# Kernel tuning notes

Hardware: AMD Instinct MI355X
Metric: run time of the kernel (lower is better)

Reference implementation:

```python
import jax, jax.numpy as jnp
import numpy as np

B, S, H, V, MAXLEN = 32, 128, 512, 32000, 64


def setup_inputs() -> dict:
    key = jax.random.key(0)
    ks = jax.random.split(key, 10)
    s = 0.05
    return {
        "word_level_rep": jax.random.normal(ks[0], (B, S, H), jnp.float32),
        "sentence_level_rep": jax.random.normal(ks[1], (B, H), jnp.float32),
        "W2": jax.random.normal(ks[2], (H,), jnp.float32) * s,          # Linear(H,1,bias=False)
        "W4": jax.random.normal(ks[3], (H, 2 * H), jnp.float32) * s,    # Linear(2H,H,bias=False), torch layout [out,in]
        "W_ih": jax.random.normal(ks[4], (4 * H, H), jnp.float32) * s,  # LSTM gates i,f,g,o
        "W_hh": jax.random.normal(ks[5], (4 * H, H), jnp.float32) * s,
        "b_ih": jax.random.normal(ks[6], (4 * H,), jnp.float32) * s,
        "b_hh": jax.random.normal(ks[7], (4 * H,), jnp.float32) * s,
        "W_out": jax.random.normal(ks[8], (V, H), jnp.float32) * s,
        "b_out": jax.random.normal(ks[9], (V,), jnp.float32) * s,
        "max_len": MAXLEN,
    }


def reference(word_level_rep, sentence_level_rep, W2, W4, W_ih, W_hh, b_ih, b_hh, W_out, b_out, max_len):
    b, seq, h_dim = word_level_rep.shape

    def step(carry, _):
        h, c = carry
        # sentence-level attention over a singleton memory bank -> weight == 1
        sent_ctx = sentence_level_rep                                   # [B,H]
        # word-level Bahdanau attention
        scores = jnp.tanh(word_level_rep + h[:, None, :]) @ W2          # [B,S]
        attn = jax.nn.softmax(scores, axis=1)                           # [B,S]
        word_ctx = jnp.einsum('bs,bsh->bh', attn, word_level_rep)       # [B,H]
        x = jnp.tanh(jnp.concatenate([sent_ctx, word_ctx], axis=-1) @ W4.T)  # [B,H]
        # PyTorch LSTM cell: gates order i, f, g, o
        gates = x @ W_ih.T + b_ih + h @ W_hh.T + b_hh                   # [B,4H]
        i, f, g, o = jnp.split(gates, 4, axis=-1)
        c_new = jax.nn.sigmoid(f) * c + jax.nn.sigmoid(i) * jnp.tanh(g)
        h_new = jax.nn.sigmoid(o) * jnp.tanh(c_new)
        out = h_new @ W_out.T + b_out                                   # [B,V]
        return (h_new, c_new), out

    h0 = jnp.zeros((b, h_dim), word_level_rep.dtype)
    c0 = jnp.zeros((b, h_dim), word_level_rep.dtype)
    (h_fin, _), outs = jax.lax.scan(step, (h0, c0), None, length=max_len)
    generated_sequence = jnp.transpose(outs, (1, 0, 2))                 # [B,max_len,V]
    return generated_sequence, h_fin
```

## Files before the change

### kernel.cpp

```cpp
#include <hip/hip_runtime.h>
#include <stdint.h>

typedef unsigned short ushort_t;
typedef unsigned long long ull_t;
typedef __attribute__((ext_vector_type(8))) short bf16x8;
typedef __attribute__((ext_vector_type(8))) unsigned short u16x8;
typedef __attribute__((ext_vector_type(4))) unsigned short u16x4;
typedef __attribute__((ext_vector_type(4))) float f32x4;

#define DEV static __device__ __forceinline__
#define SCOPE_AGENT __HIP_MEMORY_SCOPE_AGENT

DEV unsigned short f2bf(float f) {
  unsigned u = __float_as_uint(f);
  u += 0x7FFFu + ((u >> 16) & 1u);
  return (unsigned short)(u >> 16);
}
DEV float bf2f(unsigned short h) { return __uint_as_float(((unsigned)h) << 16); }
DEV float fast_rcp(float x) { return __builtin_amdgcn_rcpf(x); }
DEV float fast_tanh(float x) { float e = __expf(2.f * x); return (e - 1.f) * fast_rcp(e + 1.f); }
DEV float fast_sigm(float x) { return fast_rcp(1.f + __expf(-x)); }

DEV float wave_sum(float v) {
#pragma unroll
  for (int d = 32; d > 0; d >>= 1) v += __shfl_xor(v, d, 64);
  return v;
}
DEV float wave_max(float v) {
#pragma unroll
  for (int d = 32; d > 0; d >>= 1) v = fmaxf(v, __shfl_xor(v, d, 64));
  return v;
}

DEV void async_g2l(const void* g, void* l) {
  __builtin_amdgcn_global_load_lds((const __attribute__((address_space(1))) void*)g,
                                   (__attribute__((address_space(3))) void*)l, 16, 0, 0);
}

DEV unsigned ld_flag(unsigned* p) { return __hip_atomic_load(p, __ATOMIC_RELAXED, SCOPE_AGENT); }
DEV void st_flag(unsigned* p, unsigned v) { __hip_atomic_store(p, v, __ATOMIC_RELAXED, SCOPE_AGENT); }
DEV ull_t ld_u64(ull_t* p) { return __hip_atomic_load(p, __ATOMIC_RELAXED, SCOPE_AGENT); }
DEV void st_u64(ull_t* p, ull_t v) { __hip_atomic_store(p, v, __ATOMIC_RELAXED, SCOPE_AGENT); }
DEV void release_fence() { __builtin_amdgcn_s_waitcnt(0); }

__global__ void k_f2bf(const float* __restrict__ in, ushort_t* __restrict__ out, int n4) {
  int i = blockIdx.x * blockDim.x + threadIdx.x;
  int st = gridDim.x * blockDim.x;
  for (; i < n4; i += st) {
    f32x4 v = *(const f32x4*)(in + (size_t)i * 4);
    u16x4 o;
    o[0] = f2bf(v[0]); o[1] = f2bf(v[1]); o[2] = f2bf(v[2]); o[3] = f2bf(v[3]);
    *(u16x4*)(out + (size_t)i * 4) = o;
  }
}

__global__ __launch_bounds__(256) void k_initP(
    const float* __restrict__ w, const float* __restrict__ sent,
    const float* __restrict__ W4, ushort_t* __restrict__ P, float* __restrict__ sp)
{
  __shared__ float As2[16 * 68];
  __shared__ float Bs2[16 * 68];
  const int tid = threadIdx.x;
  const int m0 = blockIdx.x * 64, n0 = blockIdx.y * 64;
  const int tm = tid & 15, tn = tid >> 4;
  const bool sent_half = (m0 >= 4096);
  float acc[4][4];
#pragma unroll
  for (int i = 0; i < 4; i++)
#pragma unroll
    for (int j = 0; j < 4; j++) acc[i][j] = 0.f;

  for (int k0 = 0; k0 < 512; k0 += 16) {
#pragma unroll
    for (int i = 0; i < 4; i++) {
      int idx = i * 256 + tid;
      int r = idx >> 4, kk = idx & 15;
      int m = m0 + r;
      float va = 0.f;
      if (m < 4096) va = w[(size_t)m * 512 + k0 + kk];
      else if (m < 4128) va = sent[(m - 4096) * 512 + k0 + kk];
      As2[kk * 68 + r] = va;
      Bs2[kk * 68 + r] = W4[(size_t)(n0 + r) * 1024 + (sent_half ? 0 : 512) + k0 + kk];
    }
    __syncthreads();
#pragma unroll
    for (int k = 0; k < 16; k++) {
      f32x4 av = *(const f32x4*)&As2[k * 68 + tm * 4];
      f32x4 bv = *(const f32x4*)&Bs2[k * 68 + tn * 4];
#pragma unroll
      for (int i = 0; i < 4; i++)
#pragma unroll
        for (int j = 0; j < 4; j++) acc[i][j] = fmaf(av[i], bv[j], acc[i][j]);
    }
    __syncthreads();
  }
#pragma unroll
  for (int i = 0; i < 4; i++) {
    int m = m0 + tm * 4 + i;
    if (m >= 4128) continue;
#pragma unroll
    for (int j = 0; j < 4; j++) {
      int n = n0 + tn * 4 + j;
      if (m < 4096) P[(size_t)m * 512 + n] = f2bf(acc[i][j]);
      else sp[(m - 4096) * 512 + n] = acc[i][j];
    }
  }
}

struct GateS {
  ushort_t XHx[32 * 520];
  float gredf[8 * 512];
  float gates[32 * 17];
  float bias[16];
  float cstate[128];
  ushort_t hs16[128];
};
struct AttnS {
  float hs[512];
  float sps[512];
  float sc[128];
  float attw[128];
  float xpart[1024];
  ushort_t xs16[512];
};

__global__ __launch_bounds__(512) void k_recur(
    const float* __restrict__ W2, const float* __restrict__ W_ih, const float* __restrict__ W_hh,
    const float* __restrict__ b_ih, const float* __restrict__ b_hh,
    const ushort_t* __restrict__ w_bf, const ushort_t* __restrict__ P, const float* __restrict__ sp,
    unsigned* hflag, unsigned* xflag, ull_t* hbuf, ull_t* xbuf,
    ull_t* __restrict__ h_A, float* __restrict__ h_fin)
{
  __shared__ union { GateS g; AttnS a; } sm;
  const int bid = blockIdx.x, tid = threadIdx.x;
  const int wv = tid >> 6, lane = tid & 63;

  if (bid < 128) {
    const int n16 = lane & 15, quad = lane >> 4;
    const int grow = (n16 >> 2) * 512 + (bid << 2) + (n16 & 3);
    if (tid < 128) sm.g.cstate[tid] = 0.f;
    if (tid < 16) {
      int gr = (tid >> 2) * 512 + (bid << 2) + (tid & 3);
      sm.g.bias[tid] = b_ih[gr] + b_hh[gr];
    }
    bf16x8 fih[2], fhh[2];
#pragma unroll
    for (int ks = 0; ks < 2; ks++) {
      int kk = (wv * 2 + ks) * 32 + quad * 8;
      const float* pi = W_ih + (size_t)grow * 512 + kk;
      const float* ph = W_hh + (size_t)grow * 512 + kk;
#pragma unroll
      for (int j = 0; j < 8; j++) {
        fih[ks][j] = (short)f2bf(pi[j]);
        fhh[ks][j] = (short)f2bf(ph[j]);
      }
    }
    __syncthreads();

    for (int t = 0; t < 64; t++) {
      if (t > 0 && tid < 128) {
        while (ld_flag(&hflag[tid]) < (unsigned)t) __builtin_amdgcn_s_sleep(2);
      }
      __syncthreads();
      ull_t* hsrc = hbuf + ((t + 1) & 1) * 4096;
#pragma unroll
      for (int i = 0; i < 8; i++) {
        int fl = i * 512 + tid;
        ull_t v = ld_u64(&hsrc[fl]);
        *(ull_t*)&sm.g.XHx[(fl >> 7) * 520 + (fl & 127) * 4] = v;
      }
      __syncthreads();
      f32x4 acc0 = {0.f, 0.f, 0.f, 0.f}, acc1 = {0.f, 0.f, 0.f, 0.f};
#pragma unroll
      for (int ks = 0; ks < 2; ks++) {
        int kk = (wv * 2 + ks) * 32 + quad * 8;
        bf16x8 a0 = *(const bf16x8*)&sm.g.XHx[n16 * 520 + kk];
        bf16x8 a1 = *(const bf16x8*)&sm.g.XHx[(16 + n16) * 520 + kk];
        acc0 = __builtin_amdgcn_mfma_f32_16x16x32_bf16(a0, fhh[ks], acc0, 0, 0, 0);
        acc1 = __builtin_amdgcn_mfma_f32_16x16x32_bf16(a1, fhh[ks], acc1, 0, 0, 0);
      }
      if (tid < 32) {
        while (ld_flag(&xflag[tid]) < (unsigned)(t + 1)) __builtin_amdgcn_s_sleep(2);
      }
      __syncthreads();
#pragma unroll
      for (int i = 0; i < 8; i++) {
        int fl = i * 512 + tid;
        ull_t v = ld_u64(&xbuf[fl]);
        *(ull_t*)&sm.g.XHx[(fl >> 7) * 520 + (fl & 127) * 4] = v;
      }
      __syncthreads();
#pragma unroll
      for (int ks = 0; ks < 2; ks++) {
        int kk = (wv * 2 + ks) * 32 + quad * 8;
        bf16x8 a0 = *(const bf16x8*)&sm.g.XHx[n16 * 520 + kk];
        bf16x8 a1 = *(const bf16x8*)&sm.g.XHx[(16 + n16) * 520 + kk];
        acc0 = __builtin_amdgcn_mfma_f32_16x16x32_bf16(a0, fih[ks], acc0, 0, 0, 0);
        acc1 = __builtin_amdgcn_mfma_f32_16x16x32_bf16(a1, fih[ks], acc1, 0, 0, 0);
      }
      *(f32x4*)&sm.g.gredf[wv * 512 + lane * 4] = acc0;
      *(f32x4*)&sm.g.gredf[wv * 512 + 256 + lane * 4] = acc1;
      __syncthreads();
      {
        float v = 0.f;
#pragma unroll
        for (int k = 0; k < 8; k++) v += sm.g.gredf[k * 512 + tid];
        int mt = tid >> 8, l = (tid >> 2) & 63, r = tid & 3;
        int batch = mt * 16 + ((l >> 4) << 2) + r;
        int n = l & 15;
        sm.g.gates[batch * 17 + n] = v + sm.g.bias[n];
      }
      __syncthreads();
      if (tid < 128) {
        int bb = tid & 31, hr = tid >> 5;
        float gi = sm.g.gates[bb * 17 + hr];
        float gf = sm.g.gates[bb * 17 + 4 + hr];
        float gg = sm.g.gates[bb * 17 + 8 + hr];
        float go = sm.g.gates[bb * 17 + 12 + hr];
        float cold = sm.g.cstate[(bb << 2) + hr];
        float cn = fast_sigm(gf) * cold + fast_sigm(gi) * fast_tanh(gg);
        float hn = fast_sigm(go) * fast_tanh(cn);
        sm.g.cstate[(bb << 2) + hr] = cn;
        sm.g.hs16[(bb << 2) + hr] = f2bf(hn);
        if (t == 63) h_fin[bb * 512 + (bid << 2) + hr] = hn;
      }
      __syncthreads();
      if (tid < 32) {
        ull_t v = *(const ull_t*)&sm.g.hs16[tid << 2];
        st_u64(&hbuf[(t & 1) * 4096 + tid * 128 + bid], v);
        h_A[((tid << 6) + t) * 128 + bid] = v;
        release_fence();
      }
      __syncthreads();
      if (tid == 0) st_flag(&hflag[bid], (unsigned)(t + 1));
    }
  } else {
    const int b = bid - 128;
    float w2v[8];
#pragma unroll
    for (int j = 0; j < 8; j++) w2v[j] = W2[lane * 8 + j];
    sm.a.sps[tid] = sp[b * 512 + tid];
    __syncthreads();

    for (int t = 0; t < 64; t++) {
      if (t > 0 && tid < 128) {
        while (ld_flag(&hflag[tid]) < (unsigned)t) __builtin_amdgcn_s_sleep(2);
      }
      __syncthreads();
      if (tid < 128) {
        ull_t v = ld_u64(&hbuf[((t + 1) & 1) * 4096 + b * 128 + tid]);
        sm.a.hs[tid * 4 + 0] = bf2f((unsigned short)v);
        sm.a.hs[tid * 4 + 1] = bf2f((unsigned short)(v >> 16));
        sm.a.hs[tid * 4 + 2] = bf2f((unsigned short)(v >> 32));
        sm.a.hs[tid * 4 + 3] = bf2f((unsigned short)(v >> 48));
      }
      __syncthreads();
      float hf[8];
#pragma unroll
      for (int j = 0; j < 8; j++) hf[j] = sm.a.hs[lane * 8 + j];
#pragma unroll
      for (int i = 0; i < 16; i++) {
        int s = wv * 16 + i;
        u16x8 wvv = *(const u16x8*)(w_bf + ((size_t)((b << 7) + s) << 9) + lane * 8);
        float acc = 0.f;
#pragma unroll
        for (int j = 0; j < 8; j++) {
          float v = bf2f(wvv[j]) + hf[j];
          float e = __expf(2.f * v);
          acc = fmaf((e - 1.f) * fast_rcp(e + 1.f), w2v[j], acc);
        }
        acc = wave_sum(acc);
        if (lane == 0) sm.a.sc[s] = acc;
      }
      __syncthreads();
      if (wv == 0) {
        float a0 = sm.a.sc[lane], a1 = sm.a.sc[lane + 64];
        float m = wave_max(fmaxf(a0, a1));
        float e0 = __expf(a0 - m), e1 = __expf(a1 - m);
        float inv = fast_rcp(wave_sum(e0 + e1));
        sm.a.attw[lane] = e0 * inv;
        sm.a.attw[lane + 64] = e1 * inv;
      }
      __syncthreads();
      {
        int half = tid >> 8, rp = tid & 255;
        float a0 = 0.f, a1 = 0.f;
        const ushort_t* Pb = P + (((size_t)(b << 7) + half * 64) << 9) + rp * 2;
#pragma unroll 8
        for (int ss = 0; ss < 64; ss++) {
          float aw = sm.a.attw[half * 64 + ss];
          unsigned pv = *(const unsigned*)&Pb[(size_t)ss << 9];
          a0 = fmaf(aw, bf2f((unsigned short)pv), a0);
          a1 = fmaf(aw, bf2f((unsigned short)(pv >> 16)), a1);
        }
        sm.a.xpart[half * 512 + rp * 2] = a0;
        sm.a.xpart[half * 512 + rp * 2 + 1] = a1;
      }
      __syncthreads();
      {
        float xv = fast_tanh(sm.a.xpart[tid] + sm.a.xpart[512 + tid] + sm.a.sps[tid]);
        sm.a.xs16[tid] = f2bf(xv);
      }
      __syncthreads();
      if (tid < 128) {
        ull_t v = *(const ull_t*)&sm.a.xs16[tid << 2];
        st_u64(&xbuf[b * 128 + tid], v);
        release_fence();
      }
      __syncthreads();
      if (tid == 0) st_flag(&xflag[b], (unsigned)(t + 1));
    }
  }
}

__global__ __launch_bounds__(256) void k_gemm(
    const ushort_t* __restrict__ A, const ushort_t* __restrict__ Bw,
    const float* __restrict__ bias, float* __restrict__ C)
{
  __shared__ ushort_t As[128 * 64];
  __shared__ ushort_t Bs[128 * 64];
  const int tid = threadIdx.x;
  const int wave = tid >> 6, lane = tid & 63;
  const int ln = lane & 15, quad = lane >> 4;
  const int bm = blockIdx.x & 15, bn = blockIdx.x >> 4;
  const int wm = wave & 1, wn = wave >> 1;

  f32x4 acc[4][4];
#pragma unroll
  for (int i = 0; i < 4; i++)
#pragma unroll
    for (int j = 0; j < 4; j++) { acc[i][j][0] = 0.f; acc[i][j][1] = 0.f; acc[i][j][2] = 0.f; acc[i][j][3] = 0.f; }

  for (int kt = 0; kt < 8; kt++) {
    const int k0 = kt * 64;
#pragma unroll
    for (int i = 0; i < 4; i++) {
      int s = i * 256 + tid;
      int r = s >> 3, c = s & 7;
      int cs = c ^ (r & 7);
      async_g2l(A + ((size_t)(bm * 128 + r) << 9) + k0 + (cs << 3), &As[s << 3]);
    }
#pragma unroll
    for (int i = 0; i < 4; i++) {
      int s = i * 256 + tid;
      int r = s >> 3, c = s & 7;
      int cs = c ^ (r & 7);
      async_g2l(Bw + ((size_t)(bn * 128 + r) << 9) + k0 + (cs << 3), &Bs[s << 3]);
    }
    __syncthreads();
#pragma unroll
    for (int ks = 0; ks < 2; ks++) {
      bf16x8 af[4], bfr[4];
      int cc = ks * 4 + quad;
#pragma unroll
      for (int f = 0; f < 4; f++) {
        int ra = wm * 64 + f * 16 + ln;
        af[f] = *(const bf16x8*)&As[((ra << 3) + (cc ^ (ra & 7))) << 3];
        int rb = wn * 64 + f * 16 + ln;
        bfr[f] = *(const bf16x8*)&Bs[((rb << 3) + (cc ^ (rb & 7))) << 3];
      }
#pragma unroll
      for (int mf = 0; mf < 4; mf++)
#pragma unroll
        for (int nf = 0; nf < 4; nf++)
          acc[mf][nf] = __builtin_amdgcn_mfma_f32_16x16x32_bf16(af[mf], bfr[nf], acc[mf][nf], 0, 0, 0);
    }
    __syncthreads();
  }
#pragma unroll
  for (int nf = 0; nf < 4; nf++) {
    int n = bn * 128 + wn * 64 + nf * 16 + ln;
    float bv = bias[n];
#pragma unroll
    for (int mf = 0; mf < 4; mf++) {
      int mbase = bm * 128 + wm * 64 + mf * 16 + (quad << 2);
#pragma unroll
      for (int r = 0; r < 4; r++)
        C[(size_t)(mbase + r) * 32000 + n] = acc[mf][nf][r] + bv;
    }
  }
}

extern "C" void kernel_launch(void* const* d_in, const int* in_sizes, int n_in,
                              void* d_out, int out_size, void* d_ws, size_t ws_size,
                              hipStream_t stream) {
  const float* word  = (const float*)d_in[0];
  const float* sent  = (const float*)d_in[1];
  const float* W2    = (const float*)d_in[2];
  const float* W4    = (const float*)d_in[3];
  const float* W_ih  = (const float*)d_in[4];
  const float* W_hh  = (const float*)d_in[5];
  const float* b_ih  = (const float*)d_in[6];
  const float* b_hh  = (const float*)d_in[7];
  const float* W_out = (const float*)d_in[8];
  const float* b_out = (const float*)d_in[9];
  float* out = (float*)d_out;

  char* ws = (char*)d_ws;
  unsigned* hflag   = (unsigned*)(ws + 0);
  unsigned* xflag   = (unsigned*)(ws + 512);
  ull_t*    hbuf    = (ull_t*)(ws + 1024);
  ull_t*    xbuf    = (ull_t*)(ws + 66560);
  float*    sp      = (float*)(ws + 99328);
  ushort_t* P       = (ushort_t*)(ws + 164864);
  ushort_t* w_bf    = (ushort_t*)(ws + 4359168);
  ull_t*    h_A     = (ull_t*)(ws + 8553472);
  ushort_t* Wout_bf = (ushort_t*)(ws + 10650624);
  float* h_fin = out + 65536000;

  hipMemsetAsync(ws, 0, 66560, stream);

  k_f2bf<<<2048, 256, 0, stream>>>(W_out, Wout_bf, 16384000 / 4);
  k_f2bf<<<512, 256, 0, stream>>>(word, w_bf, 2097152 / 4);
  k_initP<<<dim3(65, 8), 256, 0, stream>>>(word, sent, W4, P, sp);
  k_recur<<<160, 512, 0, stream>>>(W2, W_ih, W_hh, b_ih, b_hh, w_bf, P, sp,
                                   hflag, xflag, hbuf, xbuf, h_A, h_fin);
  k_gemm<<<4000, 256, 0, stream>>>((const ushort_t*)h_A, Wout_bf, b_out, out);
}
```

Before: 1.692 ms.

## Consolidate LSTM gate blocks to 16 and overlap W_out conversion with recurrence

```diff
diff --git a/kernel.cpp b/kernel.cpp
--- a/kernel.cpp
+++ b/kernel.cpp
@@ -7,6 +7,7 @@
 typedef __attribute__((ext_vector_type(8))) unsigned short u16x8;
 typedef __attribute__((ext_vector_type(4))) unsigned short u16x4;
 typedef __attribute__((ext_vector_type(4))) float f32x4;
+typedef __attribute__((ext_vector_type(4))) unsigned u32x4;
 
 #define DEV static __device__ __forceinline__
 #define SCOPE_AGENT __HIP_MEMORY_SCOPE_AGENT
@@ -39,20 +40,15 @@
 
 DEV unsigned ld_flag(unsigned* p) { return __hip_atomic_load(p, __ATOMIC_RELAXED, SCOPE_AGENT); }
 DEV void st_flag(unsigned* p, unsigned v) { __hip_atomic_store(p, v, __ATOMIC_RELAXED, SCOPE_AGENT); }
-DEV ull_t ld_u64(ull_t* p) { return __hip_atomic_load(p, __ATOMIC_RELAXED, SCOPE_AGENT); }
 DEV void st_u64(ull_t* p, ull_t v) { __hip_atomic_store(p, v, __ATOMIC_RELAXED, SCOPE_AGENT); }
 DEV void release_fence() { __builtin_amdgcn_s_waitcnt(0); }
 
-__global__ void k_f2bf(const float* __restrict__ in, ushort_t* __restrict__ out, int n4) {
-  int i = blockIdx.x * blockDim.x + threadIdx.x;
-  int st = gridDim.x * blockDim.x;
-  for (; i < n4; i += st) {
-    f32x4 v = *(const f32x4*)(in + (size_t)i * 4);
-    u16x4 o;
-    o[0] = f2bf(v[0]); o[1] = f2bf(v[1]); o[2] = f2bf(v[2]); o[3] = f2bf(v[3]);
-    *(u16x4*)(out + (size_t)i * 4) = o;
-  }
-}
+DEV u32x4 ld_coh16(const void* p) {
+  u32x4 v;
+  asm volatile("global_load_dwordx4 %0, %1, off sc0 sc1" : "=v"(v) : "v"(p));
+  return v;
+}
+DEV void wait_vm0() { asm volatile("s_waitcnt vmcnt(0)" ::: "memory"); }
 
 __global__ __launch_bounds__(256) void k_initP(
     const float* __restrict__ w, const float* __restrict__ sent,
@@ -108,47 +104,59 @@
 }
 
 struct GateS {
-  ushort_t XHx[32 * 520];
-  float gredf[8 * 512];
-  float gates[32 * 17];
-  float bias[16];
-  float cstate[128];
-  ushort_t hs16[128];
+  ushort_t XH[32 * 520];
+  float gates[32 * 132];
+  float bias[128];
+  float cstate[1024];
+  ushort_t hs16[1024];
 };
 struct AttnS {
   float hs[512];
   float sps[512];
   float sc[128];
   float attw[128];
-  float xpart[1024];
+  float xpart[8 * 520];
   ushort_t xs16[512];
 };
 
-__global__ __launch_bounds__(512) void k_recur(
+__global__ __launch_bounds__(512, 2) void k_recur(
     const float* __restrict__ W2, const float* __restrict__ W_ih, const float* __restrict__ W_hh,
     const float* __restrict__ b_ih, const float* __restrict__ b_hh,
-    const ushort_t* __restrict__ w_bf, const ushort_t* __restrict__ P, const float* __restrict__ sp,
+    const float* __restrict__ word, const ushort_t* __restrict__ P, const float* __restrict__ sp,
     unsigned* hflag, unsigned* xflag, ull_t* hbuf, ull_t* xbuf,
-    ull_t* __restrict__ h_A, float* __restrict__ h_fin)
+    ull_t* __restrict__ h_A, float* __restrict__ h_fin,
+    const float* __restrict__ W_out, ushort_t* __restrict__ Wout_bf)
 {
   __shared__ union { GateS g; AttnS a; } sm;
   const int bid = blockIdx.x, tid = threadIdx.x;
   const int wv = tid >> 6, lane = tid & 63;
 
-  if (bid < 128) {
-    const int n16 = lane & 15, quad = lane >> 4;
-    const int grow = (n16 >> 2) * 512 + (bid << 2) + (n16 & 3);
-    if (tid < 128) sm.g.cstate[tid] = 0.f;
-    if (tid < 16) {
-      int gr = (tid >> 2) * 512 + (bid << 2) + (tid & 3);
+  if (bid >= 48) {
+    int idx = (bid - 48) * 512 + tid;
+    const int stp = (256 - 48) * 512;
+    for (; idx < 4096000; idx += stp) {
+      f32x4 v = *(const f32x4*)(W_out + (size_t)idx * 4);
+      u16x4 o;
+      o[0] = f2bf(v[0]); o[1] = f2bf(v[1]); o[2] = f2bf(v[2]); o[3] = f2bf(v[3]);
+      *(u16x4*)(Wout_bf + (size_t)idx * 4) = o;
+    }
+    return;
+  }
+
+  if (bid < 16) {
+    const int ln = lane & 15, quad = lane >> 4;
+    const int grow = (wv >> 1) * 512 + (bid << 5) + ((wv & 1) << 4) + ln;
+    sm.g.cstate[tid] = 0.f;
+    sm.g.cstate[tid + 512] = 0.f;
+    if (tid < 128) {
+      int gr = (tid >> 5) * 512 + (bid << 5) + (tid & 31);
       sm.g.bias[tid] = b_ih[gr] + b_hh[gr];
     }
-    bf16x8 fih[2], fhh[2];
-#pragma unroll
-    for (int ks = 0; ks < 2; ks++) {
-      int kk = (wv * 2 + ks) * 32 + quad * 8;
-      const float* pi = W_ih + (size_t)grow * 512 + kk;
-      const float* ph = W_hh + (size_t)grow * 512 + kk;
+    bf16x8 fih[16], fhh[16];
+#pragma unroll
+    for (int ks = 0; ks < 16; ks++) {
+      const float* pi = W_ih + (size_t)grow * 512 + ks * 32 + quad * 8;
+      const float* ph = W_hh + (size_t)grow * 512 + ks * 32 + quad * 8;
 #pragma unroll
       for (int j = 0; j < 8; j++) {
         fih[ks][j] = (short)f2bf(pi[j]);
@@ -157,85 +165,85 @@
     }
     __syncthreads();
 
+#define STAGE_XH(SRC)                                                         \
+    {                                                                         \
+      const char* src_ = (const char*)(SRC);                                  \
+      u32x4 r0 = ld_coh16(src_ + (tid << 4));                                 \
+      u32x4 r1 = ld_coh16(src_ + ((512 + tid) << 4));                         \
+      u32x4 r2 = ld_coh16(src_ + ((1024 + tid) << 4));                        \
+      u32x4 r3 = ld_coh16(src_ + ((1536 + tid) << 4));                        \
+      wait_vm0();                                                             \
+      int c1 = 512 + tid, c2 = 1024 + tid, c3 = 1536 + tid;                   \
+      *(u32x4*)&sm.g.XH[(tid >> 6) * 520 + (tid & 63) * 8] = r0;              \
+      *(u32x4*)&sm.g.XH[(c1 >> 6) * 520 + (c1 & 63) * 8] = r1;                \
+      *(u32x4*)&sm.g.XH[(c2 >> 6) * 520 + (c2 & 63) * 8] = r2;                \
+      *(u32x4*)&sm.g.XH[(c3 >> 6) * 520 + (c3 & 63) * 8] = r3;                \
+    }
+
+#define GATE_MFMA(FW)                                                         \
+    _Pragma("unroll")                                                         \
+    for (int ks = 0; ks < 16; ks++) {                                         \
+      bf16x8 a0 = *(const bf16x8*)&sm.g.XH[ln * 520 + ks * 32 + quad * 8];    \
+      bf16x8 a1 = *(const bf16x8*)&sm.g.XH[(16 + ln) * 520 + ks * 32 + quad * 8]; \
+      acc0 = __builtin_amdgcn_mfma_f32_16x16x32_bf16(a0, FW[ks], acc0, 0, 0, 0);  \
+      acc1 = __builtin_amdgcn_mfma_f32_16x16x32_bf16(a1, FW[ks], acc1, 0, 0, 0);  \
+    }
+
     for (int t = 0; t < 64; t++) {
-      if (t > 0 && tid < 128) {
-        while (ld_flag(&hflag[tid]) < (unsigned)t) __builtin_amdgcn_s_sleep(2);
-      }
-      __syncthreads();
-      ull_t* hsrc = hbuf + ((t + 1) & 1) * 4096;
-#pragma unroll
-      for (int i = 0; i < 8; i++) {
-        int fl = i * 512 + tid;
-        ull_t v = ld_u64(&hsrc[fl]);
-        *(ull_t*)&sm.g.XHx[(fl >> 7) * 520 + (fl & 127) * 4] = v;
-      }
+      if (t > 0 && tid < 16) {
+        while (ld_flag(&hflag[tid]) < (unsigned)t) __builtin_amdgcn_s_sleep(1);
+      }
+      __syncthreads();
+      STAGE_XH(hbuf + ((t + 1) & 1) * 4096);
       __syncthreads();
       f32x4 acc0 = {0.f, 0.f, 0.f, 0.f}, acc1 = {0.f, 0.f, 0.f, 0.f};
-#pragma unroll
-      for (int ks = 0; ks < 2; ks++) {
-        int kk = (wv * 2 + ks) * 32 + quad * 8;
-        bf16x8 a0 = *(const bf16x8*)&sm.g.XHx[n16 * 520 + kk];
-        bf16x8 a1 = *(const bf16x8*)&sm.g.XHx[(16 + n16) * 520 + kk];
-        acc0 = __builtin_amdgcn_mfma_f32_16x16x32_bf16(a0, fhh[ks], acc0, 0, 0, 0);
-        acc1 = __builtin_amdgcn_mfma_f32_16x16x32_bf16(a1, fhh[ks], acc1, 0, 0, 0);
-      }
+      GATE_MFMA(fhh)
       if (tid < 32) {
-        while (ld_flag(&xflag[tid]) < (unsigned)(t + 1)) __builtin_amdgcn_s_sleep(2);
-      }
-      __syncthreads();
-#pragma unroll
-      for (int i = 0; i < 8; i++) {
-        int fl = i * 512 + tid;
-        ull_t v = ld_u64(&xbuf[fl]);
-        *(ull_t*)&sm.g.XHx[(fl >> 7) * 520 + (fl & 127) * 4] = v;
-      }
-      __syncthreads();
-#pragma unroll
-      for (int ks = 0; ks < 2; ks++) {
-        int kk = (wv * 2 + ks) * 32 + quad * 8;
-        bf16x8 a0 = *(const bf16x8*)&sm.g.XHx[n16 * 520 + kk];
-        bf16x8 a1 = *(const bf16x8*)&sm.g.XHx[(16 + n16) * 520 + kk];
-        acc0 = __builtin_amdgcn_mfma_f32_16x16x32_bf16(a0, fih[ks], acc0, 0, 0, 0);
-        acc1 = __builtin_amdgcn_mfma_f32_16x16x32_bf16(a1, fih[ks], acc1, 0, 0, 0);
-      }
-      *(f32x4*)&sm.g.gredf[wv * 512 + lane * 4] = acc0;
-      *(f32x4*)&sm.g.gredf[wv * 512 + 256 + lane * 4] = acc1;
-      __syncthreads();
+        while (ld_flag(&xflag[tid]) < (unsigned)(t + 1)) __builtin_amdgcn_s_sleep(1);
+      }
+      __syncthreads();
+      STAGE_XH(xbuf);
+      __syncthreads();
+      GATE_MFMA(fih)
       {
-        float v = 0.f;
-#pragma unroll
-        for (int k = 0; k < 8; k++) v += sm.g.gredf[k * 512 + tid];
-        int mt = tid >> 8, l = (tid >> 2) & 63, r = tid & 3;
-        int batch = mt * 16 + ((l >> 4) << 2) + r;
-        int n = l & 15;
-        sm.g.gates[batch * 17 + n] = v + sm.g.bias[n];
-      }
-      __syncthreads();
-      if (tid < 128) {
-        int bb = tid & 31, hr = tid >> 5;
-        float gi = sm.g.gates[bb * 17 + hr];
-        float gf = sm.g.gates[bb * 17 + 4 + hr];
-        float gg = sm.g.gates[bb * 17 + 8 + hr];
-        float go = sm.g.gates[bb * 17 + 12 + hr];
-        float cold = sm.g.cstate[(bb << 2) + hr];
+        float bb = sm.g.bias[wv * 16 + ln];
+#pragma unroll
+        for (int reg = 0; reg < 4; reg++) {
+          sm.g.gates[(quad * 4 + reg) * 132 + wv * 16 + ln] = acc0[reg] + bb;
+          sm.g.gates[(16 + quad * 4 + reg) * 132 + wv * 16 + ln] = acc1[reg] + bb;
+        }
+      }
+      __syncthreads();
+#pragma unroll
+      for (int i = 0; i < 2; i++) {
+        int e = i * 512 + tid;
+        int b = e >> 5, hd = e & 31;
+        float gi = sm.g.gates[b * 132 + hd];
+        float gf = sm.g.gates[b * 132 + 32 + hd];
+        float gg = sm.g.gates[b * 132 + 64 + hd];
+        float go = sm.g.gates[b * 132 + 96 + hd];
+        float cold = sm.g.cstate[e];
         float cn = fast_sigm(gf) * cold + fast_sigm(gi) * fast_tanh(gg);
         float hn = fast_sigm(go) * fast_tanh(cn);
-        sm.g.cstate[(bb << 2) + hr] = cn;
-        sm.g.hs16[(bb << 2) + hr] = f2bf(hn);
-        if (t == 63) h_fin[bb * 512 + (bid << 2) + hr] = hn;
-      }
-      __syncthreads();
-      if (tid < 32) {
-        ull_t v = *(const ull_t*)&sm.g.hs16[tid << 2];
-        st_u64(&hbuf[(t & 1) * 4096 + tid * 128 + bid], v);
-        h_A[((tid << 6) + t) * 128 + bid] = v;
+        sm.g.cstate[e] = cn;
+        sm.g.hs16[e] = f2bf(hn);
+        if (t == 63) h_fin[b * 512 + (bid << 5) + hd] = hn;
+      }
+      __syncthreads();
+      if (tid < 256) {
+        int b = tid >> 3, j = tid & 7;
+        ull_t v = *(const ull_t*)&sm.g.hs16[(b << 5) + (j << 2)];
+        st_u64(&hbuf[(t & 1) * 4096 + (b << 7) + (bid << 3) + j], v);
+        h_A[(size_t)((b << 6) + t) * 128 + (bid << 3) + j] = v;
         release_fence();
       }
       __syncthreads();
       if (tid == 0) st_flag(&hflag[bid], (unsigned)(t + 1));
     }
+#undef STAGE_XH
+#undef GATE_MFMA
   } else {
-    const int b = bid - 128;
+    const int b = bid - 16;
     float w2v[8];
 #pragma unroll
     for (int j = 0; j < 8; j++) w2v[j] = W2[lane * 8 + j];
@@ -243,34 +251,44 @@
     __syncthreads();
 
     for (int t = 0; t < 64; t++) {
-      if (t > 0 && tid < 128) {
-        while (ld_flag(&hflag[tid]) < (unsigned)t) __builtin_amdgcn_s_sleep(2);
-      }
-      __syncthreads();
-      if (tid < 128) {
-        ull_t v = ld_u64(&hbuf[((t + 1) & 1) * 4096 + b * 128 + tid]);
-        sm.a.hs[tid * 4 + 0] = bf2f((unsigned short)v);
-        sm.a.hs[tid * 4 + 1] = bf2f((unsigned short)(v >> 16));
-        sm.a.hs[tid * 4 + 2] = bf2f((unsigned short)(v >> 32));
-        sm.a.hs[tid * 4 + 3] = bf2f((unsigned short)(v >> 48));
+      if (t > 0 && tid < 16) {
+        while (ld_flag(&hflag[tid]) < (unsigned)t) __builtin_amdgcn_s_sleep(1);
+      }
+      __syncthreads();
+      if (tid < 64) {
+        u32x4 hv = ld_coh16((const char*)(hbuf + ((t + 1) & 1) * 4096) + b * 1024 + (tid << 4));
+        wait_vm0();
+#pragma unroll
+        for (int j = 0; j < 4; j++) {
+          sm.a.hs[tid * 8 + 2 * j]     = bf2f((ushort_t)(hv[j] & 0xffffu));
+          sm.a.hs[tid * 8 + 2 * j + 1] = bf2f((ushort_t)(hv[j] >> 16));
+        }
       }
       __syncthreads();
       float hf[8];
 #pragma unroll
       for (int j = 0; j < 8; j++) hf[j] = sm.a.hs[lane * 8 + j];
-#pragma unroll
+      const float* wbase = word + (((size_t)b * 128 + wv * 16) << 9) + lane * 8;
+#pragma unroll 2
       for (int i = 0; i < 16; i++) {
-        int s = wv * 16 + i;
-        u16x8 wvv = *(const u16x8*)(w_bf + ((size_t)((b << 7) + s) << 9) + lane * 8);
+        const float* wp = wbase + ((size_t)i << 9);
+        f32x4 wa = *(const f32x4*)wp;
+        f32x4 wb = *(const f32x4*)(wp + 4);
         float acc = 0.f;
 #pragma unroll
-        for (int j = 0; j < 8; j++) {
-          float v = bf2f(wvv[j]) + hf[j];
-          float e = __expf(2.f * v);
+        for (int j = 0; j < 4; j++) {
+          float v = wa[j] + hf[j];
+          float e = __expf(v + v);
           acc = fmaf((e - 1.f) * fast_rcp(e + 1.f), w2v[j], acc);
         }
+#pragma unroll
+        for (int j = 0; j < 4; j++) {
+          float v = wb[j] + hf[4 + j];
+          float e = __expf(v + v);
+          acc = fmaf((e - 1.f) * fast_rcp(e + 1.f), w2v[4 + j], acc);
+        }
         acc = wave_sum(acc);
-        if (lane == 0) sm.a.sc[s] = acc;
+        if (lane == 0) sm.a.sc[wv * 16 + i] = acc;
       }
       __syncthreads();
       if (wv == 0) {
@@ -283,28 +301,31 @@
       }
       __syncthreads();
       {
-        int half = tid >> 8, rp = tid & 255;
-        float a0 = 0.f, a1 = 0.f;
-        const ushort_t* Pb = P + (((size_t)(b << 7) + half * 64) << 9) + rp * 2;
-#pragma unroll 8
-        for (int ss = 0; ss < 64; ss++) {
-          float aw = sm.a.attw[half * 64 + ss];
-          unsigned pv = *(const unsigned*)&Pb[(size_t)ss << 9];
-          a0 = fmaf(aw, bf2f((unsigned short)pv), a0);
-          a1 = fmaf(aw, bf2f((unsigned short)(pv >> 16)), a1);
+        f32x4 xacc0 = {0.f, 0.f, 0.f, 0.f}, xacc1 = {0.f, 0.f, 0.f, 0.f};
+        const ushort_t* Pb = P + (((size_t)b * 128 + wv * 16) << 9) + lane * 8;
+#pragma unroll 4
+        for (int i = 0; i < 16; i++) {
+          float aw = sm.a.attw[wv * 16 + i];
+          u16x8 pv = *(const u16x8*)(Pb + ((size_t)i << 9));
+#pragma unroll
+          for (int j = 0; j < 4; j++) xacc0[j] = fmaf(aw, bf2f(pv[j]), xacc0[j]);
+#pragma unroll
+          for (int j = 0; j < 4; j++) xacc1[j] = fmaf(aw, bf2f(pv[4 + j]), xacc1[j]);
         }
-        sm.a.xpart[half * 512 + rp * 2] = a0;
-        sm.a.xpart[half * 512 + rp * 2 + 1] = a1;
+        *(f32x4*)&sm.a.xpart[wv * 520 + lane * 8] = xacc0;
+        *(f32x4*)&sm.a.xpart[wv * 520 + lane * 8 + 4] = xacc1;
       }
       __syncthreads();
       {
-        float xv = fast_tanh(sm.a.xpart[tid] + sm.a.xpart[512 + tid] + sm.a.sps[tid]);
-        sm.a.xs16[tid] = f2bf(xv);
+        float xv = sm.a.sps[tid];
+#pragma unroll
+        for (int g = 0; g < 8; g++) xv += sm.a.xpart[g * 520 + tid];
+        sm.a.xs16[tid] = f2bf(fast_tanh(xv));
       }
       __syncthreads();
       if (tid < 128) {
         ull_t v = *(const ull_t*)&sm.a.xs16[tid << 2];
-        st_u64(&xbuf[b * 128 + tid], v);
+        st_u64(&xbuf[(b << 7) + tid], v);
         release_fence();
       }
       __syncthreads();
@@ -403,17 +424,14 @@
   ull_t*    xbuf    = (ull_t*)(ws + 66560);
   float*    sp      = (float*)(ws + 99328);
   ushort_t* P       = (ushort_t*)(ws + 164864);
-  ushort_t* w_bf    = (ushort_t*)(ws + 4359168);
   ull_t*    h_A     = (ull_t*)(ws + 8553472);
   ushort_t* Wout_bf = (ushort_t*)(ws + 10650624);
   float* h_fin = out + 65536000;
 
   hipMemsetAsync(ws, 0, 66560, stream);
 
-  k_f2bf<<<2048, 256, 0, stream>>>(W_out, Wout_bf, 16384000 / 4);
-  k_f2bf<<<512, 256, 0, stream>>>(word, w_bf, 2097152 / 4);
   k_initP<<<dim3(65, 8), 256, 0, stream>>>(word, sent, W4, P, sp);
-  k_recur<<<160, 512, 0, stream>>>(W2, W_ih, W_hh, b_ih, b_hh, w_bf, P, sp,
-                                   hflag, xflag, hbuf, xbuf, h_A, h_fin);
+  k_recur<<<256, 512, 0, stream>>>(W2, W_ih, W_hh, b_ih, b_hh, word, P, sp,
+                                   hflag, xflag, hbuf, xbuf, h_A, h_fin, W_out, Wout_bf);
   k_gemm<<<4000, 256, 0, stream>>>((const ushort_t*)h_A, Wout_bf, b_out, out);
 }
```

New measurement: 1.778 ms. 5.0% more time.

## Rewrite attention score via sigmoid identity and defer wave reductions to LDS

Applied to the files above, without the earlier changes.

```diff
diff --git a/kernel.cpp b/kernel.cpp
--- a/kernel.cpp
+++ b/kernel.cpp
@@ -43,13 +43,14 @@
 DEV void st_u64(ull_t* p, ull_t v) { __hip_atomic_store(p, v, __ATOMIC_RELAXED, SCOPE_AGENT); }
 DEV void release_fence() { __builtin_amdgcn_s_waitcnt(0); }
 
-__global__ void k_f2bf(const float* __restrict__ in, ushort_t* __restrict__ out, int n4) {
+__global__ void k_f2bf(const float* __restrict__ in, ushort_t* __restrict__ out, int n4, float scale) {
   int i = blockIdx.x * blockDim.x + threadIdx.x;
   int st = gridDim.x * blockDim.x;
   for (; i < n4; i += st) {
     f32x4 v = *(const f32x4*)(in + (size_t)i * 4);
     u16x4 o;
-    o[0] = f2bf(v[0]); o[1] = f2bf(v[1]); o[2] = f2bf(v[2]); o[3] = f2bf(v[3]);
+    o[0] = f2bf(v[0] * scale); o[1] = f2bf(v[1] * scale);
+    o[2] = f2bf(v[2] * scale); o[3] = f2bf(v[3] * scale);
     *(u16x4*)(out + (size_t)i * 4) = o;
   }
 }
@@ -118,9 +119,10 @@
 struct AttnS {
   float hs[512];
   float sps[512];
-  float sc[128];
+  float scp[128 * 68];
+  float scp4[512];
   float attw[128];
-  float xpart[1024];
+  float xpart[8 * 520];
   ushort_t xs16[512];
 };
 
@@ -239,6 +241,13 @@
     float w2v[8];
 #pragma unroll
     for (int j = 0; j < 8; j++) w2v[j] = W2[lane * 8 + j];
+    float sumW2;
+    {
+      float sw = 0.f;
+#pragma unroll
+      for (int j = 0; j < 8; j++) sw += w2v[j];
+      sumW2 = wave_sum(sw);
+    }
     sm.a.sps[tid] = sp[b * 512 + tid];
     __syncthreads();
 
@@ -249,32 +258,43 @@
       __syncthreads();
       if (tid < 128) {
         ull_t v = ld_u64(&hbuf[((t + 1) & 1) * 4096 + b * 128 + tid]);
-        sm.a.hs[tid * 4 + 0] = bf2f((unsigned short)v);
-        sm.a.hs[tid * 4 + 1] = bf2f((unsigned short)(v >> 16));
-        sm.a.hs[tid * 4 + 2] = bf2f((unsigned short)(v >> 32));
-        sm.a.hs[tid * 4 + 3] = bf2f((unsigned short)(v >> 48));
+        sm.a.hs[tid * 4 + 0] = 2.f * bf2f((unsigned short)v);
+        sm.a.hs[tid * 4 + 1] = 2.f * bf2f((unsigned short)(v >> 16));
+        sm.a.hs[tid * 4 + 2] = 2.f * bf2f((unsigned short)(v >> 32));
+        sm.a.hs[tid * 4 + 3] = 2.f * bf2f((unsigned short)(v >> 48));
       }
       __syncthreads();
       float hf[8];
 #pragma unroll
       for (int j = 0; j < 8; j++) hf[j] = sm.a.hs[lane * 8 + j];
-#pragma unroll
+#pragma unroll 4
       for (int i = 0; i < 16; i++) {
-        int s = wv * 16 + i;
-        u16x8 wvv = *(const u16x8*)(w_bf + ((size_t)((b << 7) + s) << 9) + lane * 8);
-        float acc = 0.f;
+        int s = (wv << 4) + i;
+        u16x8 wvv = *(const u16x8*)(w_bf + ((size_t)((b << 7) + s) << 9) + (lane << 3));
+        float p = 0.f;
 #pragma unroll
         for (int j = 0; j < 8; j++) {
           float v = bf2f(wvv[j]) + hf[j];
-          float e = __expf(2.f * v);
-          acc = fmaf((e - 1.f) * fast_rcp(e + 1.f), w2v[j], acc);
+          float e = __expf(v);
+          p = fmaf(w2v[j], fast_rcp(1.f + e), p);
         }
-        acc = wave_sum(acc);
-        if (lane == 0) sm.a.sc[s] = acc;
+        sm.a.scp[s * 68 + lane] = p;
+      }
+      __syncthreads();
+      {
+        int s = tid >> 2, q = tid & 3;
+        const float* pp = &sm.a.scp[s * 68 + q * 16];
+        float r = 0.f;
+#pragma unroll
+        for (int m = 0; m < 16; m++) r += pp[m];
+        sm.a.scp4[tid] = r;
       }
       __syncthreads();
       if (wv == 0) {
-        float a0 = sm.a.sc[lane], a1 = sm.a.sc[lane + 64];
+        f32x4 p0 = *(const f32x4*)&sm.a.scp4[lane * 4];
+        f32x4 p1 = *(const f32x4*)&sm.a.scp4[256 + lane * 4];
+        float a0 = sumW2 - 2.f * (p0[0] + p0[1] + p0[2] + p0[3]);
+        float a1 = sumW2 - 2.f * (p1[0] + p1[1] + p1[2] + p1[3]);
         float m = wave_max(fmaxf(a0, a1));
         float e0 = __expf(a0 - m), e1 = __expf(a1 - m);
         float inv = fast_rcp(wave_sum(e0 + e1));
@@ -283,28 +303,31 @@
       }
       __syncthreads();
       {
-        int half = tid >> 8, rp = tid & 255;
-        float a0 = 0.f, a1 = 0.f;
-        const ushort_t* Pb = P + (((size_t)(b << 7) + half * 64) << 9) + rp * 2;
-#pragma unroll 8
-        for (int ss = 0; ss < 64; ss++) {
-          float aw = sm.a.attw[half * 64 + ss];
-          unsigned pv = *(const unsigned*)&Pb[(size_t)ss << 9];
-          a0 = fmaf(aw, bf2f((unsigned short)pv), a0);
-          a1 = fmaf(aw, bf2f((unsigned short)(pv >> 16)), a1);
+        f32x4 xacc0 = {0.f, 0.f, 0.f, 0.f}, xacc1 = {0.f, 0.f, 0.f, 0.f};
+        const ushort_t* Pb = P + (((size_t)b * 128 + (wv << 4)) << 9) + lane * 8;
+#pragma unroll 4
+        for (int i = 0; i < 16; i++) {
+          float aw = sm.a.attw[(wv << 4) + i];
+          u16x8 pv = *(const u16x8*)(Pb + ((size_t)i << 9));
+#pragma unroll
+          for (int j = 0; j < 4; j++) xacc0[j] = fmaf(aw, bf2f(pv[j]), xacc0[j]);
+#pragma unroll
+          for (int j = 0; j < 4; j++) xacc1[j] = fmaf(aw, bf2f(pv[4 + j]), xacc1[j]);
         }
-        sm.a.xpart[half * 512 + rp * 2] = a0;
-        sm.a.xpart[half * 512 + rp * 2 + 1] = a1;
+        *(f32x4*)&sm.a.xpart[wv * 520 + lane * 8] = xacc0;
+        *(f32x4*)&sm.a.xpart[wv * 520 + lane * 8 + 4] = xacc1;
       }
       __syncthreads();
       {
-        float xv = fast_tanh(sm.a.xpart[tid] + sm.a.xpart[512 + tid] + sm.a.sps[tid]);
-        sm.a.xs16[tid] = f2bf(xv);
+        float xv = sm.a.sps[tid];
+#pragma unroll
+        for (int g = 0; g < 8; g++) xv += sm.a.xpart[g * 520 + tid];
+        sm.a.xs16[tid] = f2bf(fast_tanh(xv));
       }
       __syncthreads();
       if (tid < 128) {
         ull_t v = *(const ull_t*)&sm.a.xs16[tid << 2];
-        st_u64(&xbuf[b * 128 + tid], v);
+        st_u64(&xbuf[(b << 7) + tid], v);
         release_fence();
       }
       __syncthreads();
@@ -410,8 +433,8 @@
 
   hipMemsetAsync(ws, 0, 66560, stream);
 
-  k_f2bf<<<2048, 256, 0, stream>>>(W_out, Wout_bf, 16384000 / 4);
-  k_f2bf<<<512, 256, 0, stream>>>(word, w_bf, 2097152 / 4);
+  k_f2bf<<<2048, 256, 0, stream>>>(W_out, Wout_bf, 16384000 / 4, 1.0f);
+  k_f2bf<<<512, 256, 0, stream>>>(word, w_bf, 2097152 / 4, 2.0f);
   k_initP<<<dim3(65, 8), 256, 0, stream>>>(word, sent, W4, P, sp);
   k_recur<<<160, 512, 0, stream>>>(W2, W_ih, W_hh, b_ih, b_hh, w_bf, P, sp,
                                    hflag, xflag, hbuf, xbuf, h_A, h_fin);
```

Result: faster. 1.578 ms (-6.7%).
